# Kernel tuning notes

Hardware: AMD Instinct MI355X
Metric: run time of the kernel (lower is better)

The kernel has to match this reference:

```python
import jax, jax.numpy as jnp
import numpy as np
from jax import lax

B, S, T, H, VIN, VOUT = 32, 128, 64, 512, 32000, 32000
PAD_IDX = 1


def setup_inputs() -> dict:
    key = jax.random.key(0)
    ks = jax.random.split(key, 20)
    sc = 0.05
    rn = lambda k, shp: (jax.random.normal(k, shp, jnp.float32) * sc)
    return {
        "src": jax.random.randint(ks[0], (B, S), 0, VIN),
        "src_len": jnp.full((B,), S, dtype=jnp.int32),
        "trg": jax.random.randint(ks[1], (B, T), 0, VOUT),
        "enc_emb": rn(ks[2], (VIN, H)),
        "enc_wih": rn(ks[3], (4 * H, H)),
        "enc_whh": rn(ks[4], (4 * H, H)),
        "enc_bih": rn(ks[5], (4 * H,)),
        "enc_bhh": rn(ks[6], (4 * H,)),
        "enc_fc_w": rn(ks[7], (H, H)),
        "enc_fc_b": rn(ks[8], (H,)),
        "dec_emb": rn(ks[9], (VOUT, H)),
        "attn_w": rn(ks[10], (H, 2 * H)),
        "attn_b": rn(ks[11], (H,)),
        "attn_v": rn(ks[12], (H,)),
        "dec_wih": rn(ks[13], (4 * H, 2 * H)),
        "dec_whh": rn(ks[14], (4 * H, H)),
        "dec_bih": rn(ks[15], (4 * H,)),
        "dec_bhh": rn(ks[16], (4 * H,)),
        "out_w": rn(ks[17], (VOUT, 3 * H)),
        "out_b": rn(ks[18], (VOUT,)),
    }


def _lstm_cell(x, h, c, wih, whh, bih, bhh):
    # PyTorch gate order: i, f, g, o
    g = x @ wih.T + bih + h @ whh.T + bhh
    i, f, gg, o = jnp.split(g, 4, axis=-1)
    c = jax.nn.sigmoid(f) * c + jax.nn.sigmoid(i) * jnp.tanh(gg)
    h = jax.nn.sigmoid(o) * jnp.tanh(c)
    return h, c


def reference(src, src_len, trg, enc_emb, enc_wih, enc_whh, enc_bih, enc_bhh,
              enc_fc_w, enc_fc_b, dec_emb, attn_w, attn_b, attn_v,
              dec_wih, dec_whh, dec_bih, dec_bhh, out_w, out_b):
    b = src.shape[0]
    # ---- Encoder: single-layer LSTM over time (full lengths) ----
    emb = enc_emb[src].transpose(1, 0, 2)  # [S,B,H] time-major
    h0 = jnp.zeros((b, H), emb.dtype)
    c0 = jnp.zeros((b, H), emb.dtype)

    def enc_step(carry, x_t):
        h, c = carry
        h, c = _lstm_cell(x_t, h, c, enc_wih, enc_whh, enc_bih, enc_bhh)
        return (h, c), h

    (hf, cf), enc_out = lax.scan(enc_step, (h0, c0), emb)  # enc_out [S,B,H]
    hidden = jnp.tanh(hf @ enc_fc_w.T + enc_fc_b)  # [B,H]
    enc_bt = enc_out.transpose(1, 0, 2)  # [B,S,H]
    mask = src != PAD_IDX  # [B,S]

    # ---- Decoder: teacher forcing (ratio=1.0), scan over target steps ----
    def dec_step(carry, tok):
        h, c = carry
        e = dec_emb[tok]  # [B,H]
        # Bahdanau attention
        hrep = jnp.broadcast_to(h[:, None, :], enc_bt.shape)  # [B,S,H]
        energy = jnp.tanh(jnp.concatenate([hrep, enc_bt], -1) @ attn_w.T + attn_b)
        score = energy @ attn_v  # [B,S]
        score = jnp.where(mask, score, jnp.float32(-1e10))
        a = jax.nn.softmax(score, axis=1)
        weighted = jnp.einsum('bs,bsh->bh', a, enc_bt)  # [B,H]
        x = jnp.concatenate([e, weighted], -1)  # [B,2H]
        h, c = _lstm_cell(x, h, c, dec_wih, dec_whh, dec_bih, dec_bhh)
        pred = jnp.concatenate([h, weighted, e], -1) @ out_w.T + out_b  # [B,V]
        return (h, c), pred

    tokens = trg.T  # [T,B]
    (_, _), logits = lax.scan(dec_step, (hidden, cf), tokens[:-1])  # [T-1,B,V]
    outputs = jnp.concatenate(
        [jnp.zeros((1, b, VOUT), logits.dtype), logits], axis=0)  # [T,B,V]
    return outputs
```

## Files before the change

### kernel.cpp

```cpp
#include <hip/hip_runtime.h>

typedef unsigned short u16;
typedef unsigned int u32;
typedef unsigned long long u64;
typedef __attribute__((ext_vector_type(8))) short bf16x8;
typedef __attribute__((ext_vector_type(8))) unsigned short u16x8;
typedef __attribute__((ext_vector_type(4))) unsigned short u16x4;
typedef __attribute__((ext_vector_type(4))) float f32x4;

#define DEVI static __device__ __forceinline__

constexpr int B = 32, S = 128, T = 64, H = 512, V = 32000;
constexpr int H4 = 4 * H;
constexpr int TD = T - 1;
constexpr int MOUT = TD * B;
constexpr int KOUT = 3 * H;
constexpr int PAD_IDX = 1;

DEVI u16 f2bf(float f) {
  union { float f; unsigned u; } v; v.f = f;
  unsigned r = (v.u + 0x7fffu + ((v.u >> 16) & 1u)) >> 16;
  return (u16)r;
}
DEVI float bf2f(u16 h) {
  union { unsigned u; float f; } v; v.u = ((unsigned)h) << 16;
  return v.f;
}
DEVI float sigm(float x) { return 1.f / (1.f + __expf(-x)); }
DEVI float tanh_(float x) {
  float ax = fabsf(x);
  float e = __expf(-2.f * ax);
  float t = (1.f - e) / (1.f + e);
  return x < 0.f ? -t : t;
}
DEVI float tanhf_(float x) {
  float e = __expf(2.f * x);
  return 1.f - 2.f * __builtin_amdgcn_rcpf(e + 1.f);
}
DEVI int swz(int row, int k8) { return row * 32 + ((k8 ^ (row & 3)) << 3); }

DEVI u64 pack4u(const u16* p) {
  return (u64)p[0] | ((u64)p[1] << 16) | ((u64)p[2] << 32) | ((u64)p[3] << 48);
}
DEVI u64 xstore(u16* p, u64 v) {
  return __hip_atomic_exchange((u64*)p, v, __ATOMIC_RELAXED,
                               __HIP_MEMORY_SCOPE_AGENT);
}
DEVI void sstore(unsigned* p, unsigned v) {
  __hip_atomic_exchange(p, v, __ATOMIC_RELAXED, __HIP_MEMORY_SCOPE_AGENT);
}
DEVI void poll_slot(unsigned* p, unsigned tgt) {
  long long t0 = (long long)__builtin_amdgcn_s_memrealtime();
  while (__hip_atomic_load(p, __ATOMIC_RELAXED, __HIP_MEMORY_SCOPE_AGENT) <
         tgt) {
    __builtin_amdgcn_s_sleep(1);
    if ((long long)__builtin_amdgcn_s_memrealtime() - t0 > 20000000ll) break;
  }
}

__global__ __launch_bounds__(256) void gemm_bt(
    const u16* __restrict__ A, int lda,
    const u16* __restrict__ Bt, int ldb,
    float* __restrict__ C, int ldc,
    const float* __restrict__ bias, int M, int K, int bf16out) {
  __shared__ u16 As[128 * 32], Bs[128 * 32];
  const int tid = threadIdx.x;
  const int m0 = blockIdx.y * 128, n0 = blockIdx.x * 128;
  const int lane = tid & 63, w = tid >> 6, wm = w >> 1, wn = w & 1;
  const int lr = lane & 15, lk = lane >> 4;
  f32x4 acc[4][4] = {};
  const int r = tid >> 1, cc = (tid & 1) * 16, k8b = (tid & 1) * 2;

  for (int k0 = 0; k0 < K; k0 += 32) {
    {
      long gr = m0 + r;
      u16x8 v0 = {}, v1 = {};
      if (gr < M) {
        const u16* s = A + gr * (long)lda + k0 + cc;
        v0 = *(const u16x8*)s;
        v1 = *(const u16x8*)(s + 8);
      }
      *(u16x8*)&As[swz(r, k8b)] = v0;
      *(u16x8*)&As[swz(r, k8b + 1)] = v1;
    }
    {
      const u16* s = Bt + (long)(n0 + r) * ldb + k0 + cc;
      u16x8 v0 = *(const u16x8*)s;
      u16x8 v1 = *(const u16x8*)(s + 8);
      *(u16x8*)&Bs[swz(r, k8b)] = v0;
      *(u16x8*)&Bs[swz(r, k8b + 1)] = v1;
    }
    __syncthreads();
    bf16x8 af[4], bfr[4];
#pragma unroll
    for (int mi = 0; mi < 4; mi++)
      af[mi] = *(const bf16x8*)&As[swz(wm * 64 + mi * 16 + lr, lk)];
#pragma unroll
    for (int ni = 0; ni < 4; ni++)
      bfr[ni] = *(const bf16x8*)&Bs[swz(wn * 64 + ni * 16 + lr, lk)];
#pragma unroll
    for (int mi = 0; mi < 4; mi++)
#pragma unroll
      for (int ni = 0; ni < 4; ni++)
        acc[mi][ni] = __builtin_amdgcn_mfma_f32_16x16x32_bf16(
            af[mi], bfr[ni], acc[mi][ni], 0, 0, 0);
    __syncthreads();
  }
#pragma unroll
  for (int ni = 0; ni < 4; ni++) {
    int col = n0 + wn * 64 + ni * 16 + lr;
    float bs = bias ? bias[col] : 0.f;
#pragma unroll
    for (int mi = 0; mi < 4; mi++) {
#pragma unroll
      for (int rr = 0; rr < 4; rr++) {
        long row = m0 + wm * 64 + mi * 16 + lk * 4 + rr;
        if (row < M) {
          float v = acc[mi][ni][rr] + bs;
          if (bf16out)
            ((u16*)C)[row * (long)ldc + col] = f2bf(v);
          else
            C[row * (long)ldc + col] = v;
        }
      }
    }
  }
}

__global__ void zero_f(float* p, long n) {
  long i = (long)blockIdx.x * 256 + threadIdx.x;
  long st = (long)gridDim.x * 256;
  for (; i < n; i += st) p[i] = 0.f;
}

__global__ void zero_u(unsigned* p, int n) {
  int i = blockIdx.x * 256 + threadIdx.x;
  if (i < n) p[i] = 0u;
}

__global__ void cast_bf(const float* __restrict__ src, u16* __restrict__ dst,
                        int ld, int off, int Csz) {
  long row = blockIdx.y;
  int col = blockIdx.x * 256 + threadIdx.x;
  dst[row * Csz + col] = f2bf(src[row * ld + off + col]);
}

__global__ void cast_bf4(const float* __restrict__ src, u16* __restrict__ dst,
                         long n4) {
  long i = (long)blockIdx.x * 256 + threadIdx.x;
  if (i >= n4) return;
  float4 v = ((const float4*)src)[i];
  u16x4 o;
  o[0] = f2bf(v.x); o[1] = f2bf(v.y); o[2] = f2bf(v.z); o[3] = f2bf(v.w);
  *(u16x4*)&dst[i * 4] = o;
}

__global__ void cast_perm(const float* __restrict__ src, int ld, int off,
                          u16* __restrict__ dst) {
  int np = blockIdx.y;
  int c = blockIdx.x * 256 + threadIdx.x;
  int g = np & 3, jH = np >> 2;
  dst[(size_t)np * H + c] = f2bf(src[(size_t)(g * H + jH) * ld + off + c]);
}

__global__ void bias_perm(const float* __restrict__ a,
                          const float* __restrict__ b, float* __restrict__ o) {
  int np = blockIdx.x * 256 + threadIdx.x;
  int g = np & 3, jH = np >> 2;
  int r = g * H + jH;
  o[np] = a[r] + b[r];
}

__global__ __launch_bounds__(256) void cast_transpose_bf(
    const float* __restrict__ src, int ld, int off, u16* __restrict__ dst,
    int R) {
  __shared__ float tile[32][33];
  int r0 = blockIdx.y * 32, c0 = blockIdx.x * 32;
  int tx = threadIdx.x & 31, ty = threadIdx.x >> 5;
#pragma unroll
  for (int i = 0; i < 32; i += 8)
    tile[ty + i][tx] = src[(long)(r0 + ty + i) * ld + off + c0 + tx];
  __syncthreads();
#pragma unroll
  for (int i = 0; i < 32; i += 8)
    dst[(long)(c0 + ty + i) * R + r0 + tx] = f2bf(tile[tx][ty + i]);
}

__global__ void gather_src_emb(const int* __restrict__ src,
                               const float* __restrict__ emb,
                               u16* __restrict__ dst) {
  int row = blockIdx.y;
  int t = row >> 5, b = row & 31;
  int c = blockIdx.x * 256 + threadIdx.x;
  int tok = src[b * S + t];
  dst[(long)row * H + c] = f2bf(emb[(long)tok * H + c]);
}

__global__ void gather_trg_emb(const int* __restrict__ trg,
                               const float* __restrict__ emb,
                               u16* __restrict__ xout) {
  int row = blockIdx.y;
  int t = row >> 5, b = row & 31;
  int c = blockIdx.x * 256 + threadIdx.x;
  int tok = trg[b * T + t];
  xout[(long)row * KOUT + 2 * H + c] = f2bf(emb[(long)tok * H + c]);
}

__global__ __launch_bounds__(128) void enc_persist(
    unsigned* fes, const float* __restrict__ whh,
    const float* __restrict__ xih_p, u16* hstep, u16* enc_bt_bf, float* cbuf) {
  const int tid = threadIdx.x, bk = blockIdx.x;
  const int wave = tid >> 6, lane = tid & 63;
  __shared__ float gs[32][16];
  __shared__ float c_s[128];
  __shared__ u16 hx[128];
  bf16x8 wf[16];
  {
    int n = lane & 15, g = n & 3, q = n >> 2;
    const float* wrow =
        whh + ((size_t)g * H + bk * 4 + q) * H + (lane >> 4) * 8;
#pragma unroll
    for (int kt = 0; kt < 16; kt++) {
      bf16x8 f;
#pragma unroll
      for (int e = 0; e < 8; e++) f[e] = (short)f2bf(wrow[kt * 32 + e]);
      wf[kt] = f;
    }
  }
  c_s[tid] = 0.f;
  for (int t = 0; t < S; t++) {
    if (t > 0) {
      poll_slot(fes + tid * 16, (unsigned)t);
      __syncthreads();
    }
    float4 xv = *(const float4*)(xih_p + ((size_t)t * B + (tid >> 2)) * H4 +
                                 (bk * 4 + (tid & 3)) * 4);
    if (t > 0) {
      const u16* hb = hstep + (size_t)t * B * H +
                      (size_t)(wave * 16 + (lane & 15)) * H + (lane >> 4) * 8;
      f32x4 acc = {};
#pragma unroll
      for (int kt = 0; kt < 16; kt++) {
        bf16x8 a = *(const bf16x8*)(hb + kt * 32);
        acc = __builtin_amdgcn_mfma_f32_16x16x32_bf16(a, wf[kt], acc, 0, 0, 0);
      }
      int n = lane & 15, r0 = (lane >> 4) * 4;
#pragma unroll
      for (int rr = 0; rr < 4; rr++) gs[wave * 16 + r0 + rr][n] = acc[rr];
    } else {
      int n = lane & 15, r0 = (lane >> 4) * 4;
#pragma unroll
      for (int rr = 0; rr < 4; rr++) gs[wave * 16 + r0 + rr][n] = 0.f;
    }
    __syncthreads();
    {
      int b = tid >> 2, q = tid & 3;
      float gi = xv.x + gs[b][q * 4 + 0];
      float gf = xv.y + gs[b][q * 4 + 1];
      float gg = xv.z + gs[b][q * 4 + 2];
      float go = xv.w + gs[b][q * 4 + 3];
      float cn = sigm(gf) * c_s[tid] + sigm(gi) * tanh_(gg);
      c_s[tid] = cn;
      float hn = sigm(go) * tanh_(cn);
      u16 h16 = f2bf(hn);
      hx[tid] = h16;
      enc_bt_bf[((size_t)b * S + t) * H + bk * 4 + q] = h16;
    }
    __syncthreads();
    u64 kp = 0;
    if (tid < 32)
      kp = xstore(hstep + (size_t)(t + 1) * B * H + (size_t)tid * H + bk * 4,
                  pack4u(&hx[tid * 4]));
    if (wave == 0) {
      asm volatile("" :: "v"(kp));
      asm volatile("s_waitcnt vmcnt(0)" ::: "memory");
      if (tid == 0) sstore(fes + bk * 16, (unsigned)(t + 1));
    }
  }
  {
    int b = tid >> 2, q = tid & 3;
    cbuf[b * H + bk * 4 + q] = c_s[tid];
  }
}

__global__ __launch_bounds__(512) void dec_persist(
    unsigned* fhs, unsigned* fws, const float* __restrict__ fc_w,
    const float* __restrict__ fc_b, const float* __restrict__ dec_wih,
    const float* __restrict__ dec_whh, const u16* __restrict__ a1T_bf,
    const float* __restrict__ attn_v, const int* __restrict__ src,
    const u16* __restrict__ hf_bf, const float* __restrict__ cbuf,
    const u16* __restrict__ epart_bf, const u16* __restrict__ enc_bt_bf,
    const float* __restrict__ eih_p, u16* hstep, u16* wstep,
    u16* __restrict__ xout_bf) {
  const int tid = threadIdx.x, bk = blockIdx.x;
  const int wave = tid >> 6, lane = tid & 63;
  __shared__ u16 Ws[16 * 1024];
  __shared__ float wsum[8][H];
  __shared__ float hs[H], hps[H];
  __shared__ float gs4[4][32][16];
  __shared__ float sc[S], red[2];
  __shared__ int smask[S];
  __shared__ float c_s[128];
  __shared__ u16 hx[128];
  for (int idx = tid; idx < 16 * 1024; idx += 512) {
    int n = idx >> 10, k = idx & 1023;
    int g = n & 3, q = n >> 2;
    int grow = g * H + bk * 4 + q;
    float v = (k < 512) ? dec_wih[(size_t)grow * (2 * H) + 512 + k]
                        : dec_whh[(size_t)grow * H + (k - 512)];
    Ws[n * 1024 + (((k >> 3) ^ (n & 7)) << 3) + (k & 7)] = f2bf(v);
  }
  if (tid < 128) c_s[tid] = cbuf[(tid >> 2) * H + bk * 4 + (tid & 3)];
  float av8[8];
  if (bk < 32) {
    if (tid < S) smask[tid] = src[bk * S + tid];
#pragma unroll
    for (int e = 0; e < 8; e++) av8[e] = attn_v[lane * 8 + e];
  }
  if (bk < 32 && wave < 2) {
    int n = lane & 15;
    const u16* hb = hf_bf + (size_t)(wave * 16 + n) * H + (lane >> 4) * 8;
    const float* frow = fc_w + (size_t)(bk * 16 + n) * H + (lane >> 4) * 8;
    f32x4 acc = {};
#pragma unroll
    for (int kt = 0; kt < 16; kt++) {
      bf16x8 a = *(const bf16x8*)(hb + kt * 32);
      bf16x8 bf;
#pragma unroll
      for (int e = 0; e < 8; e++) bf[e] = (short)f2bf(frow[kt * 32 + e]);
      acc = __builtin_amdgcn_mfma_f32_16x16x32_bf16(a, bf, acc, 0, 0, 0);
    }
    float bias = fc_b[bk * 16 + n];
    int r0 = (lane >> 4) * 4;
#pragma unroll
    for (int rr = 0; rr < 4; rr++)
      gs4[0][wave * 16 + r0 + rr][n] = tanh_(acc[rr] + bias);
  }
  __syncthreads();
  if (bk < 32) {
    u64 kp = 0;
    if (tid < 128) {
      int b = tid >> 2, qq = tid & 3;
      u16 w0 = f2bf(gs4[0][b][qq * 4 + 0]);
      u16 w1 = f2bf(gs4[0][b][qq * 4 + 1]);
      u16 w2 = f2bf(gs4[0][b][qq * 4 + 2]);
      u16 w3 = f2bf(gs4[0][b][qq * 4 + 3]);
      u64 val = (u64)w0 | ((u64)w1 << 16) | ((u64)w2 << 32) | ((u64)w3 << 48);
      kp = xstore(hstep + (size_t)b * H + bk * 16 + qq * 4, val);
    }
    if (wave < 2) {
      asm volatile("" :: "v"(kp));
      asm volatile("s_waitcnt vmcnt(0)" ::: "memory");
    }
    __syncthreads();
    if (tid == 0) sstore(fhs + bk * 16, 1u);
  }
  for (int t = 0; t < TD; t++) {
    if (tid < 128)
      poll_slot(fhs + tid * 16, (unsigned)(tid < 32 ? t + 1 : t));
    __syncthreads();
    float4 xv = {};
    if (tid < 128)
      xv = *(const float4*)(eih_p + ((size_t)t * B + (tid >> 2)) * H4 +
                            (bk * 4 + (tid & 3)) * 4);
    if (bk < 32) {
      const int b = bk;
      if (tid < 256) {
        u32 v = ((const u32*)(hstep + (size_t)t * B * H + (size_t)b * H))[tid];
        hs[2 * tid] = bf2f((u16)(v & 0xffff));
        hs[2 * tid + 1] = bf2f((u16)(v >> 16));
      }
      __syncthreads();
      {
        float p[8] = {};
        const int j0 = lane * 8;
#pragma unroll 4
        for (int kk = 0; kk < 64; kk++) {
          int k = wave * 64 + kk;
          float hk = hs[k];
          u16x8 av = *(const u16x8*)&a1T_bf[(size_t)k * H + j0];
#pragma unroll
          for (int e = 0; e < 8; e++) p[e] += hk * bf2f(av[e]);
        }
#pragma unroll
        for (int e = 0; e < 8; e++) wsum[wave][j0 + e] = p[e];
      }
      __syncthreads();
      {
        float s0 = 0.f;
#pragma unroll
        for (int w = 0; w < 8; w++) s0 += wsum[w][tid];
        hps[tid] = s0;
      }
      __syncthreads();
      {
        const int j0 = lane * 8;
        float hp8[8];
#pragma unroll
        for (int e = 0; e < 8; e++) hp8[e] = hps[j0 + e];
        for (int i = 0; i < 16; i++) {
          int s = wave * 16 + i;
          u16x8 ep = *(const u16x8*)&epart_bf[((size_t)b * S + s) * H + j0];
          float a = 0.f;
#pragma unroll
          for (int e = 0; e < 8; e++)
            a += av8[e] * tanhf_(hp8[e] + bf2f(ep[e]));
#pragma unroll
          for (int o = 32; o; o >>= 1) a += __shfl_xor(a, o);
          if (lane == 0) sc[s] = a;
        }
      }
      __syncthreads();
      if (tid < S && smask[tid] == PAD_IDX) sc[tid] = -1e10f;
      __syncthreads();
      if (tid < 64) {
        float v = fmaxf(sc[tid], sc[tid + 64]);
#pragma unroll
        for (int o = 32; o; o >>= 1) v = fmaxf(v, __shfl_xor(v, o));
        if (tid == 0) red[0] = v;
      }
      __syncthreads();
      float mx = red[0];
      if (tid < S) sc[tid] = __expf(sc[tid] - mx);
      __syncthreads();
      if (tid < 64) {
        float v = sc[tid] + sc[tid + 64];
#pragma unroll
        for (int o = 32; o; o >>= 1) v += __shfl_xor(v, o);
        if (tid == 0) red[1] = 1.f / v;
      }
      {
        float acc8[8] = {};
        const int j0 = lane * 8;
        for (int i = 0; i < 16; i++) {
          int s = wave * 16 + i;
          float pscale = sc[s];
          u16x8 ev = *(const u16x8*)&enc_bt_bf[((size_t)b * S + s) * H + j0];
#pragma unroll
          for (int e = 0; e < 8; e++) acc8[e] += pscale * bf2f(ev[e]);
        }
#pragma unroll
        for (int e = 0; e < 8; e++) wsum[wave][j0 + e] = acc8[e];
      }
      __syncthreads();
      {
        u64 kp = 0;
        if (tid < 128) {
          float inv = red[1];
          int j0 = tid * 4;
          u16x4 o;
#pragma unroll
          for (int i = 0; i < 4; i++) {
            float wj = (wsum[0][j0 + i] + wsum[1][j0 + i] + wsum[2][j0 + i] +
                        wsum[3][j0 + i] + wsum[4][j0 + i] + wsum[5][j0 + i] +
                        wsum[6][j0 + i] + wsum[7][j0 + i]) *
                       inv;
            o[i] = f2bf(wj);
          }
          *(u16x4*)&xout_bf[((size_t)t * B + b) * KOUT + H + j0] = o;
          u64 val = (u64)o[0] | ((u64)o[1] << 16) | ((u64)o[2] << 32) |
                    ((u64)o[3] << 48);
          kp = xstore(wstep + (size_t)t * B * H + (size_t)b * H + j0, val);
        }
        if (wave < 2) {
          asm volatile("" :: "v"(kp));
          asm volatile("s_waitcnt vmcnt(0)" ::: "memory");
        }
        __syncthreads();
        if (tid == 0) sstore(fws + bk * 16, (unsigned)(t + 1));
      }
    }
    if (wave < 4) {
      int p = wave >> 1, sub = wave & 1;
      int m = lane & 15, ks = lane >> 4;
      const u16* hb =
          hstep + (size_t)t * B * H + (size_t)(sub * 16 + m) * H + ks * 8;
      f32x4 acc = {};
#pragma unroll
      for (int kt = p * 8; kt < p * 8 + 8; kt++) {
        bf16x8 a = *(const bf16x8*)(hb + kt * 32);
        bf16x8 w = *(const bf16x8*)&Ws[m * 1024 +
                                       (((64 + kt * 4 + ks) ^ (m & 7)) << 3)];
        acc = __builtin_amdgcn_mfma_f32_16x16x32_bf16(a, w, acc, 0, 0, 0);
      }
      int r0 = ks * 4;
#pragma unroll
      for (int rr = 0; rr < 4; rr++) gs4[p][sub * 16 + r0 + rr][m] = acc[rr];
    }
    if (tid < 32) poll_slot(fws + tid * 16, (unsigned)(t + 1));
    __syncthreads();
    if (wave >= 4) {
      int w2 = wave - 4, p = w2 >> 1, sub = w2 & 1;
      int m = lane & 15, ks = lane >> 4;
      const u16* wb_ =
          wstep + (size_t)t * B * H + (size_t)(sub * 16 + m) * H + ks * 8;
      f32x4 acc = {};
#pragma unroll
      for (int kt = p * 8; kt < p * 8 + 8; kt++) {
        bf16x8 a = *(const bf16x8*)(wb_ + kt * 32);
        bf16x8 w =
            *(const bf16x8*)&Ws[m * 1024 + (((kt * 4 + ks) ^ (m & 7)) << 3)];
        acc = __builtin_amdgcn_mfma_f32_16x16x32_bf16(a, w, acc, 0, 0, 0);
      }
      int r0 = ks * 4;
#pragma unroll
      for (int rr = 0; rr < 4; rr++)
        gs4[2 + p][sub * 16 + r0 + rr][m] = acc[rr];
    }
    __syncthreads();
    if (tid < 128) {
      int b2 = tid >> 2, q = tid & 3;
      float gi = xv.x + gs4[0][b2][q * 4 + 0] + gs4[1][b2][q * 4 + 0] +
                 gs4[2][b2][q * 4 + 0] + gs4[3][b2][q * 4 + 0];
      float gf = xv.y + gs4[0][b2][q * 4 + 1] + gs4[1][b2][q * 4 + 1] +
                 gs4[2][b2][q * 4 + 1] + gs4[3][b2][q * 4 + 1];
      float gg = xv.z + gs4[0][b2][q * 4 + 2] + gs4[1][b2][q * 4 + 2] +
                 gs4[2][b2][q * 4 + 2] + gs4[3][b2][q * 4 + 2];
      float go = xv.w + gs4[0][b2][q * 4 + 3] + gs4[1][b2][q * 4 + 3] +
                 gs4[2][b2][q * 4 + 3] + gs4[3][b2][q * 4 + 3];
      float cn = sigm(gf) * c_s[tid] + sigm(gi) * tanh_(gg);
      c_s[tid] = cn;
      float hn = sigm(go) * tanh_(cn);
      u16 h16 = f2bf(hn);
      hx[tid] = h16;
      xout_bf[((size_t)t * B + b2) * KOUT + bk * 4 + q] = h16;
    }
    __syncthreads();
    u64 kp2 = 0;
    if (tid < 32)
      kp2 = xstore(hstep + (size_t)(t + 1) * B * H + (size_t)tid * H + bk * 4,
                   pack4u(&hx[tid * 4]));
    if (wave == 0) {
      asm volatile("" :: "v"(kp2));
      asm volatile("s_waitcnt vmcnt(0)" ::: "memory");
      if (tid == 0)
        sstore(fhs + bk * 16, (unsigned)(bk < 32 ? t + 2 : t + 1));
    }
  }
}

extern "C" void kernel_launch(void* const* d_in, const int* in_sizes, int n_in,
                              void* d_out, int out_size, void* d_ws,
                              size_t ws_size, hipStream_t stream) {
  const int* src = (const int*)d_in[0];
  const int* trg = (const int*)d_in[2];
  const float* enc_emb = (const float*)d_in[3];
  const float* enc_wih = (const float*)d_in[4];
  const float* enc_whh = (const float*)d_in[5];
  const float* enc_bih = (const float*)d_in[6];
  const float* enc_bhh = (const float*)d_in[7];
  const float* fc_w = (const float*)d_in[8];
  const float* fc_b = (const float*)d_in[9];
  const float* dec_emb = (const float*)d_in[10];
  const float* attn_w = (const float*)d_in[11];
  const float* attn_b = (const float*)d_in[12];
  const float* attn_v = (const float*)d_in[13];
  const float* dec_wih = (const float*)d_in[14];
  const float* dec_whh = (const float*)d_in[15];
  const float* dec_bih = (const float*)d_in[16];
  const float* dec_bhh = (const float*)d_in[17];
  const float* out_w = (const float*)d_in[18];
  const float* out_b = (const float*)d_in[19];
  float* out = (float*)d_out;

  char* wp = (char*)d_ws;
  auto alloc = [&](size_t n) {
    char* p = wp;
    wp += (n + 255) & ~(size_t)255;
    return p;
  };
  u16* outw_bf = (u16*)alloc((size_t)V * KOUT * 2);
  u16* wihenc_p = (u16*)alloc((size_t)H4 * H * 2);
  u16* wihE_p = (u16*)alloc((size_t)H4 * H * 2);
  u16* attnw2_bf = (u16*)alloc((size_t)H * H * 2);
  u16* a1T_bf = (u16*)alloc((size_t)H * H * 2);
  u16* xemb_bf = (u16*)alloc((size_t)S * B * H * 2);
  float* xih_p = (float*)alloc((size_t)S * B * H4 * 4);
  u16* enc_bt_bf = (u16*)alloc((size_t)B * S * H * 2);
  u16* epart_bf = (u16*)alloc((size_t)B * S * H * 2);
  float* eih_p = (float*)alloc((size_t)MOUT * H4 * 4);
  u16* xout_bf = (u16*)alloc((size_t)MOUT * KOUT * 2);
  u16* hstep_enc = (u16*)alloc((size_t)(S + 1) * B * H * 2);
  u16* hstep_dec = (u16*)alloc((size_t)T * B * H * 2);
  u16* wstep = (u16*)alloc((size_t)TD * B * H * 2);
  float* cbuf = (float*)alloc((size_t)B * H * 4);
  float* benc_p = (float*)alloc((size_t)H4 * 4);
  float* bdec_p = (float*)alloc((size_t)H4 * 4);
  unsigned* flags = (unsigned*)alloc(4608 * 4);
  unsigned* fes = flags;
  unsigned* fhs = flags + 2048;
  unsigned* fws = flags + 4096;

  dim3 blk(256);
  zero_f<<<dim3(256), blk, 0, stream>>>(out, (long)B * V);
  zero_u<<<dim3(18), blk, 0, stream>>>(flags, 4608);
  cast_bf4<<<dim3(((long)V * KOUT / 4 + 255) / 256), blk, 0, stream>>>(
      out_w, outw_bf, (long)V * KOUT / 4);
  cast_perm<<<dim3(H / 256, H4), blk, 0, stream>>>(enc_wih, H, 0, wihenc_p);
  cast_perm<<<dim3(H / 256, H4), blk, 0, stream>>>(dec_wih, 2 * H, 0, wihE_p);
  cast_bf<<<dim3(H / 256, H), blk, 0, stream>>>(attn_w, attnw2_bf, 2 * H, H, H);
  cast_transpose_bf<<<dim3(H / 32, H / 32), blk, 0, stream>>>(attn_w, 2 * H, 0,
                                                              a1T_bf, H);
  bias_perm<<<dim3(H4 / 256), blk, 0, stream>>>(enc_bih, enc_bhh, benc_p);
  bias_perm<<<dim3(H4 / 256), blk, 0, stream>>>(dec_bih, dec_bhh, bdec_p);
  gather_src_emb<<<dim3(H / 256, S * B), blk, 0, stream>>>(src, enc_emb,
                                                           xemb_bf);
  gather_trg_emb<<<dim3(H / 256, MOUT), blk, 0, stream>>>(trg, dec_emb,
                                                          xout_bf);
  gemm_bt<<<dim3(H4 / 128, (S * B) / 128), blk, 0, stream>>>(
      xemb_bf, H, wihenc_p, H, xih_p, H4, benc_p, S * B, H, 0);
  gemm_bt<<<dim3(H4 / 128, (MOUT + 127) / 128), blk, 0, stream>>>(
      xout_bf + 2 * H, KOUT, wihE_p, H, eih_p, H4, bdec_p, MOUT, H, 0);
  enc_persist<<<dim3(128), dim3(128), 0, stream>>>(fes, enc_whh, xih_p,
                                                   hstep_enc, enc_bt_bf, cbuf);
  gemm_bt<<<dim3(H / 128, (B * S) / 128), blk, 0, stream>>>(
      enc_bt_bf, H, attnw2_bf, H, (float*)epart_bf, H, attn_b, B * S, H, 1);
  dec_persist<<<dim3(128), dim3(512), 0, stream>>>(
      fhs, fws, fc_w, fc_b, dec_wih, dec_whh, a1T_bf, attn_v, src,
      hstep_enc + (size_t)S * B * H, cbuf, epart_bf, enc_bt_bf, eih_p,
      hstep_dec, wstep, xout_bf);
  gemm_bt<<<dim3(V / 128, (MOUT + 127) / 128), blk, 0, stream>>>(
      xout_bf, KOUT, outw_bf, KOUT, out + (size_t)B * V, V, out_b, MOUT, KOUT,
      0);
}
```

Before: 2.623 ms.

## Shrink persistent LSTM kernels to 32 blocks with global-memory weights

Rewrites the encoder and decoder persistent recurrent kernels to use 32 blocks of 512 threads, each owning 16 hidden units, instead of 128 blocks each owning 4. Recurrent weights are pre-packed into bf16 gate-interleaved global buffers and streamed from global memory rather than kept in registers or LDS. The decoder's recurrent GEMM is folded into all blocks, all of which also run attention. Polling uses a sleep backoff. The aim is to cut the number of blocks taking part in each per-step cross-block flag handshake and so reduce synchronisation latency, at the cost of more per-block work and repeated weight reads from L2 every step.

```diff
diff --git a/kernel.cpp b/kernel.cpp
--- a/kernel.cpp
+++ b/kernel.cpp
@@ -9,6 +9,7 @@
 typedef __attribute__((ext_vector_type(4))) float f32x4;
 
 #define DEVI static __device__ __forceinline__
+#define MFMA __builtin_amdgcn_mfma_f32_16x16x32_bf16
 
 constexpr int B = 32, S = 128, T = 64, H = 512, V = 32000;
 constexpr int H4 = 4 * H;
@@ -49,11 +50,17 @@
 DEVI void sstore(unsigned* p, unsigned v) {
   __hip_atomic_exchange(p, v, __ATOMIC_RELAXED, __HIP_MEMORY_SCOPE_AGENT);
 }
-DEVI void poll_slot(unsigned* p, unsigned tgt) {
+DEVI void poll_bo(unsigned* p, unsigned tgt) {
+  int it = 0;
   long long t0 = (long long)__builtin_amdgcn_s_memrealtime();
   while (__hip_atomic_load(p, __ATOMIC_RELAXED, __HIP_MEMORY_SCOPE_AGENT) <
          tgt) {
-    __builtin_amdgcn_s_sleep(1);
+    if (it < 4) {
+      __builtin_amdgcn_s_sleep(1);
+      it++;
+    } else {
+      __builtin_amdgcn_s_sleep(8);
+    }
     if ((long long)__builtin_amdgcn_s_memrealtime() - t0 > 20000000ll) break;
   }
 }
@@ -102,8 +109,7 @@
     for (int mi = 0; mi < 4; mi++)
 #pragma unroll
       for (int ni = 0; ni < 4; ni++)
-        acc[mi][ni] = __builtin_amdgcn_mfma_f32_16x16x32_bf16(
-            af[mi], bfr[ni], acc[mi][ni], 0, 0, 0);
+        acc[mi][ni] = MFMA(af[mi], bfr[ni], acc[mi][ni], 0, 0, 0);
     __syncthreads();
   }
 #pragma unroll
@@ -163,6 +169,18 @@
   dst[(size_t)np * H + c] = f2bf(src[(size_t)(g * H + jH) * ld + off + c]);
 }
 
+__global__ void pack_wdec_p(const float* __restrict__ wih,
+                            const float* __restrict__ whh,
+                            u16* __restrict__ dst) {
+  int r = blockIdx.y;
+  int k = blockIdx.x * 256 + threadIdx.x;
+  int g = r & 3, j = r >> 2;
+  int srow = g * H + j;
+  float v = (k < 512) ? wih[(size_t)srow * (2 * H) + 512 + k]
+                      : whh[(size_t)srow * H + (k - 512)];
+  dst[(size_t)r * 1024 + k] = f2bf(v);
+}
+
 __global__ void bias_perm(const float* __restrict__ a,
                           const float* __restrict__ b, float* __restrict__ o) {
   int np = blockIdx.x * 256 + threadIdx.x;
@@ -206,335 +224,287 @@
   xout[(long)row * KOUT + 2 * H + c] = f2bf(emb[(long)tok * H + c]);
 }
 
-__global__ __launch_bounds__(128) void enc_persist(
-    unsigned* fes, const float* __restrict__ whh,
+__global__ __launch_bounds__(512) void enc_persist32(
+    unsigned* fes, const u16* __restrict__ wenc_p,
     const float* __restrict__ xih_p, u16* hstep, u16* enc_bt_bf, float* cbuf) {
+  __shared__ float gs[32][64];
+  __shared__ float c_s[512];
+  __shared__ u16 hx[512];
   const int tid = threadIdx.x, bk = blockIdx.x;
   const int wave = tid >> 6, lane = tid & 63;
-  __shared__ float gs[32][16];
-  __shared__ float c_s[128];
-  __shared__ u16 hx[128];
-  bf16x8 wf[16];
-  {
-    int n = lane & 15, g = n & 3, q = n >> 2;
-    const float* wrow =
-        whh + ((size_t)g * H + bk * 4 + q) * H + (lane >> 4) * 8;
-#pragma unroll
-    for (int kt = 0; kt < 16; kt++) {
-      bf16x8 f;
-#pragma unroll
-      for (int e = 0; e < 8; e++) f[e] = (short)f2bf(wrow[kt * 32 + e]);
-      wf[kt] = f;
-    }
-  }
+  const int lr = lane & 15, lk = lane >> 4;
+  const int bq = tid >> 4, jl = tid & 15;
   c_s[tid] = 0.f;
+  const int mt = wave & 1, nt = wave >> 1;
+  const int n = nt * 16 + lr;
+  const u16* wp = wenc_p + (size_t)(bk * 64 + n) * 512 + lk * 8;
   for (int t = 0; t < S; t++) {
-    if (t > 0) {
-      poll_slot(fes + tid * 16, (unsigned)t);
-      __syncthreads();
-    }
-    float4 xv = *(const float4*)(xih_p + ((size_t)t * B + (tid >> 2)) * H4 +
-                                 (bk * 4 + (tid & 3)) * 4);
-    if (t > 0) {
-      const u16* hb = hstep + (size_t)t * B * H +
-                      (size_t)(wave * 16 + (lane & 15)) * H + (lane >> 4) * 8;
+    if (t > 0 && tid < 32) poll_bo(fes + tid * 16, (unsigned)t);
+    __syncthreads();
+    float4 xv = *(const float4*)(xih_p + ((size_t)t * B + bq) * H4 +
+                                 (bk * 16 + jl) * 4);
+    {
+      const u16* ab =
+          hstep + (size_t)t * B * H + (size_t)(mt * 16 + lr) * H + lk * 8;
       f32x4 acc = {};
 #pragma unroll
       for (int kt = 0; kt < 16; kt++) {
-        bf16x8 a = *(const bf16x8*)(hb + kt * 32);
-        acc = __builtin_amdgcn_mfma_f32_16x16x32_bf16(a, wf[kt], acc, 0, 0, 0);
-      }
-      int n = lane & 15, r0 = (lane >> 4) * 4;
-#pragma unroll
-      for (int rr = 0; rr < 4; rr++) gs[wave * 16 + r0 + rr][n] = acc[rr];
-    } else {
-      int n = lane & 15, r0 = (lane >> 4) * 4;
-#pragma unroll
-      for (int rr = 0; rr < 4; rr++) gs[wave * 16 + r0 + rr][n] = 0.f;
-    }
-    __syncthreads();
-    {
-      int b = tid >> 2, q = tid & 3;
-      float gi = xv.x + gs[b][q * 4 + 0];
-      float gf = xv.y + gs[b][q * 4 + 1];
-      float gg = xv.z + gs[b][q * 4 + 2];
-      float go = xv.w + gs[b][q * 4 + 3];
+        bf16x8 a = *(const bf16x8*)(ab + kt * 32);
+        bf16x8 w = *(const bf16x8*)(wp + kt * 32);
+        acc = MFMA(a, w, acc, 0, 0, 0);
+      }
+#pragma unroll
+      for (int rr = 0; rr < 4; rr++) gs[mt * 16 + lk * 4 + rr][n] = acc[rr];
+    }
+    __syncthreads();
+    {
+      float gi = xv.x + gs[bq][jl * 4 + 0];
+      float gf = xv.y + gs[bq][jl * 4 + 1];
+      float gg = xv.z + gs[bq][jl * 4 + 2];
+      float go = xv.w + gs[bq][jl * 4 + 3];
       float cn = sigm(gf) * c_s[tid] + sigm(gi) * tanh_(gg);
       c_s[tid] = cn;
-      float hn = sigm(go) * tanh_(cn);
-      u16 h16 = f2bf(hn);
+      u16 h16 = f2bf(sigm(go) * tanh_(cn));
       hx[tid] = h16;
-      enc_bt_bf[((size_t)b * S + t) * H + bk * 4 + q] = h16;
-    }
-    __syncthreads();
-    u64 kp = 0;
-    if (tid < 32)
-      kp = xstore(hstep + (size_t)(t + 1) * B * H + (size_t)tid * H + bk * 4,
-                  pack4u(&hx[tid * 4]));
-    if (wave == 0) {
-      asm volatile("" :: "v"(kp));
-      asm volatile("s_waitcnt vmcnt(0)" ::: "memory");
-      if (tid == 0) sstore(fes + bk * 16, (unsigned)(t + 1));
-    }
-  }
-  {
-    int b = tid >> 2, q = tid & 3;
-    cbuf[b * H + bk * 4 + q] = c_s[tid];
-  }
-}
-
-__global__ __launch_bounds__(512) void dec_persist(
-    unsigned* fhs, unsigned* fws, const float* __restrict__ fc_w,
-    const float* __restrict__ fc_b, const float* __restrict__ dec_wih,
-    const float* __restrict__ dec_whh, const u16* __restrict__ a1T_bf,
-    const float* __restrict__ attn_v, const int* __restrict__ src,
-    const u16* __restrict__ hf_bf, const float* __restrict__ cbuf,
-    const u16* __restrict__ epart_bf, const u16* __restrict__ enc_bt_bf,
-    const float* __restrict__ eih_p, u16* hstep, u16* wstep,
-    u16* __restrict__ xout_bf) {
-  const int tid = threadIdx.x, bk = blockIdx.x;
-  const int wave = tid >> 6, lane = tid & 63;
-  __shared__ u16 Ws[16 * 1024];
-  __shared__ float wsum[8][H];
-  __shared__ float hs[H], hps[H];
-  __shared__ float gs4[4][32][16];
-  __shared__ float sc[S], red[2];
-  __shared__ int smask[S];
-  __shared__ float c_s[128];
-  __shared__ u16 hx[128];
-  for (int idx = tid; idx < 16 * 1024; idx += 512) {
-    int n = idx >> 10, k = idx & 1023;
-    int g = n & 3, q = n >> 2;
-    int grow = g * H + bk * 4 + q;
-    float v = (k < 512) ? dec_wih[(size_t)grow * (2 * H) + 512 + k]
-                        : dec_whh[(size_t)grow * H + (k - 512)];
-    Ws[n * 1024 + (((k >> 3) ^ (n & 7)) << 3) + (k & 7)] = f2bf(v);
-  }
-  if (tid < 128) c_s[tid] = cbuf[(tid >> 2) * H + bk * 4 + (tid & 3)];
-  float av8[8];
-  if (bk < 32) {
-    if (tid < S) smask[tid] = src[bk * S + tid];
-#pragma unroll
-    for (int e = 0; e < 8; e++) av8[e] = attn_v[lane * 8 + e];
-  }
-  if (bk < 32 && wave < 2) {
-    int n = lane & 15;
-    const u16* hb = hf_bf + (size_t)(wave * 16 + n) * H + (lane >> 4) * 8;
-    const float* frow = fc_w + (size_t)(bk * 16 + n) * H + (lane >> 4) * 8;
-    f32x4 acc = {};
-#pragma unroll
-    for (int kt = 0; kt < 16; kt++) {
-      bf16x8 a = *(const bf16x8*)(hb + kt * 32);
-      bf16x8 bf;
-#pragma unroll
-      for (int e = 0; e < 8; e++) bf[e] = (short)f2bf(frow[kt * 32 + e]);
-      acc = __builtin_amdgcn_mfma_f32_16x16x32_bf16(a, bf, acc, 0, 0, 0);
-    }
-    float bias = fc_b[bk * 16 + n];
-    int r0 = (lane >> 4) * 4;
-#pragma unroll
-    for (int rr = 0; rr < 4; rr++)
-      gs4[0][wave * 16 + r0 + rr][n] = tanh_(acc[rr] + bias);
-  }
-  __syncthreads();
-  if (bk < 32) {
+      enc_bt_bf[((size_t)bq * S + t) * H + bk * 16 + jl] = h16;
+    }
+    __syncthreads();
     u64 kp = 0;
     if (tid < 128) {
-      int b = tid >> 2, qq = tid & 3;
-      u16 w0 = f2bf(gs4[0][b][qq * 4 + 0]);
-      u16 w1 = f2bf(gs4[0][b][qq * 4 + 1]);
-      u16 w2 = f2bf(gs4[0][b][qq * 4 + 2]);
-      u16 w3 = f2bf(gs4[0][b][qq * 4 + 3]);
-      u64 val = (u64)w0 | ((u64)w1 << 16) | ((u64)w2 << 32) | ((u64)w3 << 48);
-      kp = xstore(hstep + (size_t)b * H + bk * 16 + qq * 4, val);
+      int bb = tid >> 2, q = tid & 3;
+      kp = xstore(hstep + (size_t)(t + 1) * B * H + (size_t)bb * H + bk * 16 +
+                      q * 4,
+                  pack4u(&hx[bb * 16 + q * 4]));
     }
     if (wave < 2) {
       asm volatile("" :: "v"(kp));
       asm volatile("s_waitcnt vmcnt(0)" ::: "memory");
     }
     __syncthreads();
+    if (tid == 0) sstore(fes + bk * 16, (unsigned)(t + 1));
+  }
+  cbuf[bq * H + bk * 16 + jl] = c_s[tid];
+}
+
+__global__ __launch_bounds__(512) void dec_persist32(
+    unsigned* fhs, unsigned* fws, const float* __restrict__ fc_w,
+    const float* __restrict__ fc_b, const u16* __restrict__ wdec_p,
+    const u16* __restrict__ a1T_bf, const float* __restrict__ attn_v,
+    const int* __restrict__ src, const u16* __restrict__ hf_bf,
+    const float* __restrict__ cbuf, const u16* __restrict__ epart_bf,
+    const u16* __restrict__ enc_bt_bf, const float* __restrict__ eih_p,
+    u16* hstep, u16* wstep, u16* __restrict__ xout_bf) {
+  __shared__ float buf[8][512];
+  __shared__ float hs[512], hps[512];
+  __shared__ float sc[128], red[2];
+  __shared__ int smask[128];
+  __shared__ float c_s[512];
+  __shared__ u16 hx[512];
+  const int tid = threadIdx.x, bk = blockIdx.x;
+  const int wave = tid >> 6, lane = tid & 63;
+  const int lr = lane & 15, lk = lane >> 4;
+  const int bq = tid >> 4, jl = tid & 15;
+  c_s[tid] = cbuf[bq * H + bk * 16 + jl];
+  if (tid < 128) smask[tid] = src[bk * S + tid];
+  float av8[8];
+#pragma unroll
+  for (int e = 0; e < 8; e++) av8[e] = attn_v[lane * 8 + e];
+  if (wave < 2) {
+    const u16* ab = hf_bf + (size_t)(wave * 16 + lr) * H + lk * 8;
+    const float* frow = fc_w + (size_t)(bk * 16 + lr) * H + lk * 8;
+    f32x4 acc = {};
+#pragma unroll
+    for (int kt = 0; kt < 16; kt++) {
+      bf16x8 a = *(const bf16x8*)(ab + kt * 32);
+      bf16x8 w;
+#pragma unroll
+      for (int e = 0; e < 8; e++) w[e] = (short)f2bf(frow[kt * 32 + e]);
+      acc = MFMA(a, w, acc, 0, 0, 0);
+    }
+    float bs = fc_b[bk * 16 + lr];
+#pragma unroll
+    for (int rr = 0; rr < 4; rr++)
+      hx[(wave * 16 + lk * 4 + rr) * 16 + lr] = f2bf(tanh_(acc[rr] + bs));
+  }
+  __syncthreads();
+  {
+    u64 kp = 0;
+    if (tid < 128) {
+      int bb = tid >> 2, q = tid & 3;
+      kp = xstore(hstep + (size_t)bb * H + bk * 16 + q * 4,
+                  pack4u(&hx[bb * 16 + q * 4]));
+    }
+    if (wave < 2) {
+      asm volatile("" :: "v"(kp));
+      asm volatile("s_waitcnt vmcnt(0)" ::: "memory");
+    }
+    __syncthreads();
     if (tid == 0) sstore(fhs + bk * 16, 1u);
   }
+  const int mt = wave & 1, nt = wave >> 1;
+  const int n = nt * 16 + lr;
+  const u16* wpw = wdec_p + (size_t)(bk * 64 + n) * 1024 + lk * 8;
+  const u16* wph = wpw + 512;
   for (int t = 0; t < TD; t++) {
-    if (tid < 128)
-      poll_slot(fhs + tid * 16, (unsigned)(tid < 32 ? t + 1 : t));
-    __syncthreads();
-    float4 xv = {};
-    if (tid < 128)
-      xv = *(const float4*)(eih_p + ((size_t)t * B + (tid >> 2)) * H4 +
-                            (bk * 4 + (tid & 3)) * 4);
-    if (bk < 32) {
-      const int b = bk;
-      if (tid < 256) {
-        u32 v = ((const u32*)(hstep + (size_t)t * B * H + (size_t)b * H))[tid];
-        hs[2 * tid] = bf2f((u16)(v & 0xffff));
-        hs[2 * tid + 1] = bf2f((u16)(v >> 16));
+    if (tid < 32) poll_bo(fhs + tid * 16, (unsigned)(t + 1));
+    __syncthreads();
+    float4 xv = *(const float4*)(eih_p + ((size_t)t * B + bq) * H4 +
+                                 (bk * 16 + jl) * 4);
+    if (tid < 256) {
+      u32 v = ((const u32*)(hstep + (size_t)t * B * H + (size_t)bk * H))[tid];
+      hs[2 * tid] = bf2f((u16)(v & 0xffff));
+      hs[2 * tid + 1] = bf2f((u16)(v >> 16));
+    }
+    __syncthreads();
+    {
+      float p[8] = {};
+      const int j0 = lane * 8;
+#pragma unroll 4
+      for (int kk = 0; kk < 64; kk++) {
+        int k = wave * 64 + kk;
+        float hk = hs[k];
+        u16x8 av = *(const u16x8*)&a1T_bf[(size_t)k * H + j0];
+#pragma unroll
+        for (int e = 0; e < 8; e++) p[e] += hk * bf2f(av[e]);
+      }
+#pragma unroll
+      for (int e = 0; e < 8; e++) buf[wave][j0 + e] = p[e];
+    }
+    __syncthreads();
+    {
+      float s0 = 0.f;
+#pragma unroll
+      for (int w = 0; w < 8; w++) s0 += buf[w][tid];
+      hps[tid] = s0;
+    }
+    __syncthreads();
+    {
+      const int j0 = lane * 8;
+      float hp8[8];
+#pragma unroll
+      for (int e = 0; e < 8; e++) hp8[e] = hps[j0 + e];
+      for (int i = 0; i < 16; i++) {
+        int s = wave * 16 + i;
+        u16x8 ep = *(const u16x8*)&epart_bf[((size_t)bk * S + s) * H + j0];
+        float a = 0.f;
+#pragma unroll
+        for (int e = 0; e < 8; e++) a += av8[e] * tanhf_(hp8[e] + bf2f(ep[e]));
+#pragma unroll
+        for (int o = 32; o; o >>= 1) a += __shfl_xor(a, o);
+        if (lane == 0) sc[s] = (smask[s] == PAD_IDX) ? -1e10f : a;
+      }
+    }
+    __syncthreads();
+    if (tid < 64) {
+      float v = fmaxf(sc[tid], sc[tid + 64]);
+#pragma unroll
+      for (int o = 32; o; o >>= 1) v = fmaxf(v, __shfl_xor(v, o));
+      if (tid == 0) red[0] = v;
+    }
+    __syncthreads();
+    float mx = red[0];
+    if (tid < S) sc[tid] = __expf(sc[tid] - mx);
+    __syncthreads();
+    if (tid < 64) {
+      float v = sc[tid] + sc[tid + 64];
+#pragma unroll
+      for (int o = 32; o; o >>= 1) v += __shfl_xor(v, o);
+      if (tid == 0) red[1] = 1.f / v;
+    }
+    __syncthreads();
+    {
+      float acc8[8] = {};
+      const int j0 = lane * 8;
+      for (int i = 0; i < 16; i++) {
+        int s = wave * 16 + i;
+        float ps = sc[s];
+        u16x8 ev = *(const u16x8*)&enc_bt_bf[((size_t)bk * S + s) * H + j0];
+#pragma unroll
+        for (int e = 0; e < 8; e++) acc8[e] += ps * bf2f(ev[e]);
+      }
+#pragma unroll
+      for (int e = 0; e < 8; e++) buf[wave][j0 + e] = acc8[e];
+    }
+    __syncthreads();
+    {
+      u64 kp = 0;
+      if (tid < 128) {
+        float inv = red[1];
+        int j0 = tid * 4;
+        u16x4 o;
+#pragma unroll
+        for (int i = 0; i < 4; i++) {
+          float wj = (buf[0][j0 + i] + buf[1][j0 + i] + buf[2][j0 + i] +
+                      buf[3][j0 + i] + buf[4][j0 + i] + buf[5][j0 + i] +
+                      buf[6][j0 + i] + buf[7][j0 + i]) *
+                     inv;
+          o[i] = f2bf(wj);
+        }
+        *(u16x4*)&xout_bf[((size_t)t * B + bk) * KOUT + H + j0] = o;
+        u64 val = (u64)o[0] | ((u64)o[1] << 16) | ((u64)o[2] << 32) |
+                  ((u64)o[3] << 48);
+        kp = xstore(wstep + ((size_t)t * B + bk) * H + j0, val);
+      }
+      if (wave < 2) {
+        asm volatile("" :: "v"(kp));
+        asm volatile("s_waitcnt vmcnt(0)" ::: "memory");
       }
       __syncthreads();
-      {
-        float p[8] = {};
-        const int j0 = lane * 8;
-#pragma unroll 4
-        for (int kk = 0; kk < 64; kk++) {
-          int k = wave * 64 + kk;
-          float hk = hs[k];
-          u16x8 av = *(const u16x8*)&a1T_bf[(size_t)k * H + j0];
-#pragma unroll
-          for (int e = 0; e < 8; e++) p[e] += hk * bf2f(av[e]);
-        }
-#pragma unroll
-        for (int e = 0; e < 8; e++) wsum[wave][j0 + e] = p[e];
-      }
-      __syncthreads();
-      {
-        float s0 = 0.f;
-#pragma unroll
-        for (int w = 0; w < 8; w++) s0 += wsum[w][tid];
-        hps[tid] = s0;
-      }
-      __syncthreads();
-      {
-        const int j0 = lane * 8;
-        float hp8[8];
-#pragma unroll
-        for (int e = 0; e < 8; e++) hp8[e] = hps[j0 + e];
-        for (int i = 0; i < 16; i++) {
-          int s = wave * 16 + i;
-          u16x8 ep = *(const u16x8*)&epart_bf[((size_t)b * S + s) * H + j0];
-          float a = 0.f;
-#pragma unroll
-          for (int e = 0; e < 8; e++)
-            a += av8[e] * tanhf_(hp8[e] + bf2f(ep[e]));
-#pragma unroll
-          for (int o = 32; o; o >>= 1) a += __shfl_xor(a, o);
-          if (lane == 0) sc[s] = a;
-        }
-      }
-      __syncthreads();
-      if (tid < S && smask[tid] == PAD_IDX) sc[tid] = -1e10f;
-      __syncthreads();
-      if (tid < 64) {
-        float v = fmaxf(sc[tid], sc[tid + 64]);
-#pragma unroll
-        for (int o = 32; o; o >>= 1) v = fmaxf(v, __shfl_xor(v, o));
-        if (tid == 0) red[0] = v;
-      }
-      __syncthreads();
-      float mx = red[0];
-      if (tid < S) sc[tid] = __expf(sc[tid] - mx);
-      __syncthreads();
-      if (tid < 64) {
-        float v = sc[tid] + sc[tid + 64];
-#pragma unroll
-        for (int o = 32; o; o >>= 1) v += __shfl_xor(v, o);
-        if (tid == 0) red[1] = 1.f / v;
-      }
-      {
-        float acc8[8] = {};
-        const int j0 = lane * 8;
-        for (int i = 0; i < 16; i++) {
-          int s = wave * 16 + i;
-          float pscale = sc[s];
-          u16x8 ev = *(const u16x8*)&enc_bt_bf[((size_t)b * S + s) * H + j0];
-#pragma unroll
-          for (int e = 0; e < 8; e++) acc8[e] += pscale * bf2f(ev[e]);
-        }
-#pragma unroll
-        for (int e = 0; e < 8; e++) wsum[wave][j0 + e] = acc8[e];
-      }
-      __syncthreads();
-      {
-        u64 kp = 0;
-        if (tid < 128) {
-          float inv = red[1];
-          int j0 = tid * 4;
-          u16x4 o;
-#pragma unroll
-          for (int i = 0; i < 4; i++) {
-            float wj = (wsum[0][j0 + i] + wsum[1][j0 + i] + wsum[2][j0 + i] +
-                        wsum[3][j0 + i] + wsum[4][j0 + i] + wsum[5][j0 + i] +
-                        wsum[6][j0 + i] + wsum[7][j0 + i]) *
-                       inv;
-            o[i] = f2bf(wj);
-          }
-          *(u16x4*)&xout_bf[((size_t)t * B + b) * KOUT + H + j0] = o;
-          u64 val = (u64)o[0] | ((u64)o[1] << 16) | ((u64)o[2] << 32) |
-                    ((u64)o[3] << 48);
-          kp = xstore(wstep + (size_t)t * B * H + (size_t)b * H + j0, val);
-        }
-        if (wave < 2) {
-          asm volatile("" :: "v"(kp));
-          asm volatile("s_waitcnt vmcnt(0)" ::: "memory");
-        }
-        __syncthreads();
-        if (tid == 0) sstore(fws + bk * 16, (unsigned)(t + 1));
-      }
-    }
-    if (wave < 4) {
-      int p = wave >> 1, sub = wave & 1;
-      int m = lane & 15, ks = lane >> 4;
-      const u16* hb =
-          hstep + (size_t)t * B * H + (size_t)(sub * 16 + m) * H + ks * 8;
+      if (tid == 0) sstore(fws + bk * 16, (unsigned)(t + 1));
+    }
+    if (tid < 32) poll_bo(fws + tid * 16, (unsigned)(t + 1));
+    __syncthreads();
+    {
+      const u16* aw =
+          wstep + (size_t)t * B * H + (size_t)(mt * 16 + lr) * H + lk * 8;
+      const u16* ah =
+          hstep + (size_t)t * B * H + (size_t)(mt * 16 + lr) * H + lk * 8;
       f32x4 acc = {};
 #pragma unroll
-      for (int kt = p * 8; kt < p * 8 + 8; kt++) {
-        bf16x8 a = *(const bf16x8*)(hb + kt * 32);
-        bf16x8 w = *(const bf16x8*)&Ws[m * 1024 +
-                                       (((64 + kt * 4 + ks) ^ (m & 7)) << 3)];
-        acc = __builtin_amdgcn_mfma_f32_16x16x32_bf16(a, w, acc, 0, 0, 0);
-      }
-      int r0 = ks * 4;
-#pragma unroll
-      for (int rr = 0; rr < 4; rr++) gs4[p][sub * 16 + r0 + rr][m] = acc[rr];
-    }
-    if (tid < 32) poll_slot(fws + tid * 16, (unsigned)(t + 1));
-    __syncthreads();
-    if (wave >= 4) {
-      int w2 = wave - 4, p = w2 >> 1, sub = w2 & 1;
-      int m = lane & 15, ks = lane >> 4;
-      const u16* wb_ =
-          wstep + (size_t)t * B * H + (size_t)(sub * 16 + m) * H + ks * 8;
-      f32x4 acc = {};
-#pragma unroll
-      for (int kt = p * 8; kt < p * 8 + 8; kt++) {
-        bf16x8 a = *(const bf16x8*)(wb_ + kt * 32);
-        bf16x8 w =
-            *(const bf16x8*)&Ws[m * 1024 + (((kt * 4 + ks) ^ (m & 7)) << 3)];
-        acc = __builtin_amdgcn_mfma_f32_16x16x32_bf16(a, w, acc, 0, 0, 0);
-      }
-      int r0 = ks * 4;
+      for (int kt = 0; kt < 16; kt++) {
+        bf16x8 a = *(const bf16x8*)(aw + kt * 32);
+        bf16x8 w = *(const bf16x8*)(wpw + kt * 32);
+        acc = MFMA(a, w, acc, 0, 0, 0);
+      }
+#pragma unroll
+      for (int kt = 0; kt < 16; kt++) {
+        bf16x8 a = *(const bf16x8*)(ah + kt * 32);
+        bf16x8 w = *(const bf16x8*)(wph + kt * 32);
+        acc = MFMA(a, w, acc, 0, 0, 0);
+      }
+      float* gsp = &buf[0][0];
 #pragma unroll
       for (int rr = 0; rr < 4; rr++)
-        gs4[2 + p][sub * 16 + r0 + rr][m] = acc[rr];
-    }
-    __syncthreads();
-    if (tid < 128) {
-      int b2 = tid >> 2, q = tid & 3;
-      float gi = xv.x + gs4[0][b2][q * 4 + 0] + gs4[1][b2][q * 4 + 0] +
-                 gs4[2][b2][q * 4 + 0] + gs4[3][b2][q * 4 + 0];
-      float gf = xv.y + gs4[0][b2][q * 4 + 1] + gs4[1][b2][q * 4 + 1] +
-                 gs4[2][b2][q * 4 + 1] + gs4[3][b2][q * 4 + 1];
-      float gg = xv.z + gs4[0][b2][q * 4 + 2] + gs4[1][b2][q * 4 + 2] +
-                 gs4[2][b2][q * 4 + 2] + gs4[3][b2][q * 4 + 2];
-      float go = xv.w + gs4[0][b2][q * 4 + 3] + gs4[1][b2][q * 4 + 3] +
-                 gs4[2][b2][q * 4 + 3] + gs4[3][b2][q * 4 + 3];
+        gsp[(mt * 16 + lk * 4 + rr) * 64 + n] = acc[rr];
+    }
+    __syncthreads();
+    {
+      const float* gsp = &buf[0][0];
+      float gi = xv.x + gsp[bq * 64 + jl * 4 + 0];
+      float gf = xv.y + gsp[bq * 64 + jl * 4 + 1];
+      float gg = xv.z + gsp[bq * 64 + jl * 4 + 2];
+      float go = xv.w + gsp[bq * 64 + jl * 4 + 3];
       float cn = sigm(gf) * c_s[tid] + sigm(gi) * tanh_(gg);
       c_s[tid] = cn;
-      float hn = sigm(go) * tanh_(cn);
-      u16 h16 = f2bf(hn);
+      u16 h16 = f2bf(sigm(go) * tanh_(cn));
       hx[tid] = h16;
-      xout_bf[((size_t)t * B + b2) * KOUT + bk * 4 + q] = h16;
-    }
-    __syncthreads();
-    u64 kp2 = 0;
-    if (tid < 32)
-      kp2 = xstore(hstep + (size_t)(t + 1) * B * H + (size_t)tid * H + bk * 4,
-                   pack4u(&hx[tid * 4]));
-    if (wave == 0) {
-      asm volatile("" :: "v"(kp2));
-      asm volatile("s_waitcnt vmcnt(0)" ::: "memory");
-      if (tid == 0)
-        sstore(fhs + bk * 16, (unsigned)(bk < 32 ? t + 2 : t + 1));
+      xout_bf[((size_t)t * B + bq) * KOUT + bk * 16 + jl] = h16;
+    }
+    __syncthreads();
+    {
+      u64 kp = 0;
+      if (tid < 128) {
+        int bb = tid >> 2, q = tid & 3;
+        kp = xstore(hstep + (size_t)(t + 1) * B * H + (size_t)bb * H +
+                        bk * 16 + q * 4,
+                    pack4u(&hx[bb * 16 + q * 4]));
+      }
+      if (wave < 2) {
+        asm volatile("" :: "v"(kp));
+        asm volatile("s_waitcnt vmcnt(0)" ::: "memory");
+      }
+      __syncthreads();
+      if (tid == 0) sstore(fhs + bk * 16, (unsigned)(t + 2));
     }
   }
 }
@@ -572,6 +542,8 @@
   u16* outw_bf = (u16*)alloc((size_t)V * KOUT * 2);
   u16* wihenc_p = (u16*)alloc((size_t)H4 * H * 2);
   u16* wihE_p = (u16*)alloc((size_t)H4 * H * 2);
+  u16* wenc_p = (u16*)alloc((size_t)H4 * H * 2);
+  u16* wdec_p = (u16*)alloc((size_t)H4 * 2 * H * 2);
   u16* attnw2_bf = (u16*)alloc((size_t)H * H * 2);
   u16* a1T_bf = (u16*)alloc((size_t)H * H * 2);
   u16* xemb_bf = (u16*)alloc((size_t)S * B * H * 2);
@@ -586,18 +558,21 @@
   float* cbuf = (float*)alloc((size_t)B * H * 4);
   float* benc_p = (float*)alloc((size_t)H4 * 4);
   float* bdec_p = (float*)alloc((size_t)H4 * 4);
-  unsigned* flags = (unsigned*)alloc(4608 * 4);
+  unsigned* flags = (unsigned*)alloc(2048 * 4);
   unsigned* fes = flags;
-  unsigned* fhs = flags + 2048;
-  unsigned* fws = flags + 4096;
+  unsigned* fhs = flags + 512;
+  unsigned* fws = flags + 1024;
 
   dim3 blk(256);
   zero_f<<<dim3(256), blk, 0, stream>>>(out, (long)B * V);
-  zero_u<<<dim3(18), blk, 0, stream>>>(flags, 4608);
+  zero_u<<<dim3(8), blk, 0, stream>>>(flags, 2048);
+  zero_u<<<dim3(32), blk, 0, stream>>>((unsigned*)hstep_enc, B * H / 2);
   cast_bf4<<<dim3(((long)V * KOUT / 4 + 255) / 256), blk, 0, stream>>>(
       out_w, outw_bf, (long)V * KOUT / 4);
   cast_perm<<<dim3(H / 256, H4), blk, 0, stream>>>(enc_wih, H, 0, wihenc_p);
   cast_perm<<<dim3(H / 256, H4), blk, 0, stream>>>(dec_wih, 2 * H, 0, wihE_p);
+  cast_perm<<<dim3(H / 256, H4), blk, 0, stream>>>(enc_whh, H, 0, wenc_p);
+  pack_wdec_p<<<dim3(4, H4), blk, 0, stream>>>(dec_wih, dec_whh, wdec_p);
   cast_bf<<<dim3(H / 256, H), blk, 0, stream>>>(attn_w, attnw2_bf, 2 * H, H, H);
   cast_transpose_bf<<<dim3(H / 32, H / 32), blk, 0, stream>>>(attn_w, 2 * H, 0,
                                                               a1T_bf, H);
@@ -611,12 +586,12 @@
       xemb_bf, H, wihenc_p, H, xih_p, H4, benc_p, S * B, H, 0);
   gemm_bt<<<dim3(H4 / 128, (MOUT + 127) / 128), blk, 0, stream>>>(
       xout_bf + 2 * H, KOUT, wihE_p, H, eih_p, H4, bdec_p, MOUT, H, 0);
-  enc_persist<<<dim3(128), dim3(128), 0, stream>>>(fes, enc_whh, xih_p,
-                                                   hstep_enc, enc_bt_bf, cbuf);
+  enc_persist32<<<dim3(32), dim3(512), 0, stream>>>(fes, wenc_p, xih_p,
+                                                    hstep_enc, enc_bt_bf, cbuf);
   gemm_bt<<<dim3(H / 128, (B * S) / 128), blk, 0, stream>>>(
       enc_bt_bf, H, attnw2_bf, H, (float*)epart_bf, H, attn_b, B * S, H, 1);
-  dec_persist<<<dim3(128), dim3(512), 0, stream>>>(
-      fhs, fws, fc_w, fc_b, dec_wih, dec_whh, a1T_bf, attn_v, src,
+  dec_persist32<<<dim3(32), dim3(512), 0, stream>>>(
+      fhs, fws, fc_w, fc_b, wdec_p, a1T_bf, attn_v, src,
       hstep_enc + (size_t)S * B * H, cbuf, epart_bf, enc_bt_bf, eih_p,
       hstep_dec, wstep, xout_bf);
   gemm_bt<<<dim3(V / 128, (MOUT + 127) / 128), blk, 0, stream>>>(
```

Result: slower. 3.265 ms (+24.5%).
